# Kernel optimization log

Measured on AMD Instinct MI355X. Metric: run time of the kernel, lower is better.

The kernel has to match this reference:

```python
import jax, jax.numpy as jnp
import numpy as np
import math

DIM = 512
B, T, H, W = 1, 8, 64, 64


def setup_inputs() -> dict:
    key = jax.random.key(0)
    k0, k1, k2 = jax.random.split(key, 3)
    x = jax.random.normal(k0, (B, DIM, T, H, W), dtype=jnp.float32)
    gamma = jnp.ones((DIM,), jnp.float32)                      # RMS_norm gamma (viewed as flat vector)
    w_qkv = jax.random.normal(k1, (3 * DIM, DIM), jnp.float32) * 0.02  # conv1x1 weight (out, in)
    b_qkv = jnp.zeros((3 * DIM,), jnp.float32)
    w_proj = jax.random.normal(k2, (DIM, DIM), jnp.float32) * 0.02     # zero-init in torch; random for a meaningful baseline
    b_proj = jnp.zeros((DIM,), jnp.float32)
    return dict(x=x, gamma=gamma, w_qkv=w_qkv, b_qkv=b_qkv, w_proj=w_proj, b_proj=b_proj)


def reference(x, gamma, w_qkv, b_qkv, w_proj, b_proj):
    b, c, t, h, w = x.shape
    xt = jnp.transpose(x, (0, 2, 3, 4, 1))          # [b, t, h, w, c]
    identity = xt
    y = xt.reshape(b * t, h, w, c)
    # RMS_norm: L2 norm over channels (last dim), clamped, scaled by sqrt(c)*gamma
    norm = jnp.clip(jnp.linalg.norm(y, axis=-1, keepdims=True), 1e-12, None)
    y = y / norm * (c ** 0.5) * gamma
    # 1x1 conv QKV as GEMM over channels
    qkv = jnp.einsum('bhwc,oc->bhwo', y, w_qkv) + b_qkv        # [bt, h, w, 3c]
    qkv = qkv.reshape(b * t, h * w, 1, 3 * c)                  # nh=1 per source rearrange
    q, k, v = jnp.split(qkv, 3, axis=-1)                       # each [bt, hw, 1, c]
    scale = 1.0 / math.sqrt(c)
    # NOTE: hw sits in the batch position (faithful to source); seq len = nh = 1
    attn = jnp.einsum('bsnc,bsmc->bsnm', q, k) * scale         # [bt, hw, 1, 1]
    attn = jax.nn.softmax(attn, axis=-1)                       # trivially 1.0
    o = jnp.einsum('bsnm,bsmc->bsnc', attn, v)                 # == v
    o = o.reshape(b * t, h, w, c)
    o = jnp.einsum('bhwc,oc->bhwo', o, w_proj) + b_proj        # 1x1 proj conv
    o = o.reshape(b, t, h, w, c)
    out = jnp.transpose(o + identity, (0, 4, 1, 2, 3))         # back to [b, c, t, h, w]
    return out
```

## Files before the change

### kernel.cpp

```cpp
#include <hip/hip_runtime.h>

typedef unsigned short ushort_t;
typedef __attribute__((ext_vector_type(8))) short short8;
typedef __attribute__((ext_vector_type(4))) float f32x4;

#define DIMC 512
#define PN   32768
#define SQRTC 22.627416997969522f

__device__ __forceinline__ ushort_t f2bf(float f) {
  unsigned int u = __float_as_uint(f);
  unsigned int r = u + 0x7fffu + ((u >> 16) & 1u);
  return (ushort_t)(r >> 16);
}

__device__ __forceinline__ int kkey(int r) { return (r & 7) ^ ((r >> 2) & 7); }

__device__ __forceinline__ uint4 pack8(float4 a, float4 b) {
  union { ushort_t u[8]; uint4 v; } r;
  r.u[0] = f2bf(a.x); r.u[1] = f2bf(a.y); r.u[2] = f2bf(a.z); r.u[3] = f2bf(a.w);
  r.u[4] = f2bf(b.x); r.u[5] = f2bf(b.y); r.u[6] = f2bf(b.z); r.u[7] = f2bf(b.w);
  return r.v;
}

__global__ __launch_bounds__(256) void k_wgemm(
    const float* __restrict__ wproj,
    const float* __restrict__ wqkv,
    const float* __restrict__ bqkv,
    const float* __restrict__ bproj,
    const float* __restrict__ gamma,
    ushort_t* __restrict__ Mp2,
    float* __restrict__ fb) {
  int bid = blockIdx.x, tid = threadIdx.x;
  if (bid >= 16) {
    int wave = tid >> 6, lane = tid & 63;
    int o = (bid - 16) * 4 + wave;
    float part = 0.f;
#pragma unroll
    for (int i = 0; i < 8; ++i) {
      int k = lane + i * 64;
      part += wproj[o * DIMC + k] * bqkv[1024 + k];
    }
    for (int off = 32; off; off >>= 1) part += __shfl_down(part, off, 64);
    if (lane == 0) fb[o] = part + bproj[o];
    return;
  }

  __shared__ ushort_t As[128 * 64];
  __shared__ ushort_t Bs[128 * 64];
  int c0 = (bid & 3) * 128;
  int o0 = (bid >> 2) * 128;
  int wave = tid >> 6, lane = tid & 63;
  int wo = (wave & 1) * 64, wp = (wave >> 1) * 64;
  int q = lane >> 4, ln = lane & 15;

  f32x4 zero = {0.f, 0.f, 0.f, 0.f};
  f32x4 acc[4][4];
#pragma unroll
  for (int i = 0; i < 4; ++i)
#pragma unroll
    for (int j = 0; j < 4; ++j) acc[i][j] = zero;

  int sr = tid >> 3;
  int sc = tid & 7;
  const float* Ag = wproj + (long)(o0 + sr) * DIMC + sc * 8;
  int kr = tid >> 5;
  int c4 = (tid & 31) * 4;

  for (int kc = 0; kc < DIMC; kc += 64) {
    __syncthreads();
#pragma unroll
    for (int it = 0; it < 4; ++it) {
      int r = sr + it * 32;
      float4 a0 = *(const float4*)(Ag + (long)it * 32 * DIMC + kc);
      float4 a1 = *(const float4*)(Ag + (long)it * 32 * DIMC + kc + 4);
      *(uint4*)(&As[r * 64 + ((sc ^ (r & 7)) * 8)]) = pack8(a0, a1);
    }
#pragma unroll
    for (int ps = 0; ps < 8; ++ps) {
      int k = kc + ps * 8 + kr;
      float4 b = *(const float4*)(wqkv + (long)(1024 + k) * DIMC + c0 + c4);
      char* bsb = (char*)Bs;
      ushort_t e[4] = {f2bf(b.x), f2bf(b.y), f2bf(b.z), f2bf(b.w)};
#pragma unroll
      for (int i = 0; i < 4; ++i) {
        int c = c4 + i;
        *(ushort_t*)(bsb + c * 128 + ((ps ^ kkey(c)) * 16) + kr * 2) = e[i];
      }
    }
    __syncthreads();
#pragma unroll
    for (int ks = 0; ks < 2; ++ks) {
      int cch = ks * 4 + q;
      short8 af[4], bf[4];
#pragma unroll
      for (int mi = 0; mi < 4; ++mi) {
        int row = wo + mi * 16 + ln;
        af[mi] = *(const short8*)(&As[row * 64 + ((cch ^ (row & 7)) * 8)]);
      }
#pragma unroll
      for (int ni = 0; ni < 4; ++ni) {
        int row = wp + ni * 16 + ln;
        bf[ni] = *(const short8*)(&Bs[row * 64 + ((cch ^ kkey(row)) * 8)]);
      }
#pragma unroll
      for (int mi = 0; mi < 4; ++mi)
#pragma unroll
        for (int ni = 0; ni < 4; ++ni)
          acc[mi][ni] = __builtin_amdgcn_mfma_f32_16x16x32_bf16(af[mi], bf[ni], acc[mi][ni], 0, 0, 0);
    }
  }

#pragma unroll
  for (int mi = 0; mi < 4; ++mi) {
    int obase = o0 + wo + mi * 16 + q * 4;
#pragma unroll
    for (int ni = 0; ni < 4; ++ni) {
      int c = c0 + wp + ni * 16 + ln;
      float g = gamma[c];
      int kb2 = c >> 6, ks2 = (c >> 5) & 1, q2 = (c >> 3) & 3, j2 = c & 7;
#pragma unroll
      for (int r = 0; r < 4; ++r) {
        int o = obase + r;
        int w2 = o >> 6, mi2 = (o >> 4) & 3, ln2 = o & 15;
        long idx = (((((long)w2 * 8 + kb2) * 2 + ks2) * 4 + mi2) * 64 + q2 * 16 + ln2) * 8 + j2;
        Mp2[idx] = f2bf(acc[mi][ni][r] * g);
      }
    }
  }
}

__global__ __launch_bounds__(512, 4) void k_fused(
    const float* __restrict__ x,
    const ushort_t* __restrict__ Mp2,
    const float* __restrict__ fb,
    float* __restrict__ out) {
  __shared__ ushort_t xs[8 * 64 * 64];
  __shared__ float red[32 * 65];
  __shared__ float s_sh[64];
  int tid = threadIdx.x;
  long p0 = (long)blockIdx.x * 64;

  int wave = tid >> 6, lane = tid & 63;
  int q = lane >> 4, ln = lane & 15;

  int pl4 = (tid & 15) * 4;
  int kp  = tid >> 4;
  int kl  = kp * 2;
  int ch  = kl >> 3;
  int sub = (kl & 7) * 2;
  const float* xb = x + p0 + pl4;

  const ushort_t* Aw = Mp2 + (long)wave * 32768 + lane * 8;

  float ss0 = 0.f, ss1 = 0.f, ss2 = 0.f, ss3 = 0.f;
  float4 u0, u1;

#define LOADX(KB)                                                  \
  { const float* xp = xb + (long)((KB) * 64 + kl) * PN;            \
    u0 = *(const float4*)(xp);  u1 = *(const float4*)(xp + PN); }

#define SSW(KB)                                                                 \
  { ss0 += u0.x * u0.x + u1.x * u1.x;  ss1 += u0.y * u0.y + u1.y * u1.y;        \
    ss2 += u0.z * u0.z + u1.z * u1.z;  ss3 += u0.w * u0.w + u1.w * u1.w;        \
    unsigned int w0 = (unsigned int)f2bf(u0.x) | ((unsigned int)f2bf(u1.x) << 16); \
    unsigned int w1 = (unsigned int)f2bf(u0.y) | ((unsigned int)f2bf(u1.y) << 16); \
    unsigned int w2 = (unsigned int)f2bf(u0.z) | ((unsigned int)f2bf(u1.z) << 16); \
    unsigned int w3 = (unsigned int)f2bf(u0.w) | ((unsigned int)f2bf(u1.w) << 16); \
    char* bb = (char*)xs + (KB) * 8192;                                         \
    *(unsigned int*)(bb + (pl4 + 0) * 128 + ((ch ^ kkey(pl4 + 0)) * 16) + sub) = w0; \
    *(unsigned int*)(bb + (pl4 + 1) * 128 + ((ch ^ kkey(pl4 + 1)) * 16) + sub) = w1; \
    *(unsigned int*)(bb + (pl4 + 2) * 128 + ((ch ^ kkey(pl4 + 2)) * 16) + sub) = w2; \
    *(unsigned int*)(bb + (pl4 + 3) * 128 + ((ch ^ kkey(pl4 + 3)) * 16) + sub) = w3; }

  f32x4 zero = {0.f, 0.f, 0.f, 0.f};
  f32x4 acc[4][4];
#pragma unroll
  for (int i = 0; i < 4; ++i)
#pragma unroll
    for (int j = 0; j < 4; ++j) acc[i][j] = zero;

  LOADX(0); SSW(0);
  __syncthreads();

#pragma unroll
  for (int kb = 0; kb < 8; ++kb) {
    if (kb < 7) LOADX(kb + 1);
    const char* bbase = (const char*)xs + kb * 8192;
#pragma unroll
    for (int ks = 0; ks < 2; ++ks) {
      short8 af[4], bf[4];
#pragma unroll
      for (int mi = 0; mi < 4; ++mi)
        af[mi] = *(const short8*)(Aw + ((kb * 2 + ks) * 4 + mi) * 512);
      int cch = ks * 4 + q;
#pragma unroll
      for (int ni = 0; ni < 4; ++ni) {
        int row = ni * 16 + ln;
        bf[ni] = *(const short8*)(bbase + row * 128 + ((cch ^ kkey(row)) * 16));
      }
#pragma unroll
      for (int mi = 0; mi < 4; ++mi)
#pragma unroll
        for (int ni = 0; ni < 4; ++ni)
          acc[mi][ni] = __builtin_amdgcn_mfma_f32_16x16x32_bf16(af[mi], bf[ni], acc[mi][ni], 0, 0, 0);
    }
    if (kb < 7) {
      SSW(kb + 1);
      __syncthreads();
    }
  }

  red[kp * 65 + pl4 + 0] = ss0;
  red[kp * 65 + pl4 + 1] = ss1;
  red[kp * 65 + pl4 + 2] = ss2;
  red[kp * 65 + pl4 + 3] = ss3;
  __syncthreads();
  if (tid < 64) {
    float t = 0.f;
#pragma unroll
    for (int g = 0; g < 32; ++g) t += red[g * 65 + tid];
    s_sh[tid] = SQRTC / fmaxf(sqrtf(t), 1e-12f);
  }
  __syncthreads();

  int wo = wave * 64;
#pragma unroll
  for (int mi = 0; mi < 4; ++mi) {
    int obase = wo + mi * 16 + q * 4;
#pragma unroll
    for (int ni = 0; ni < 4; ++ni) {
      int plocal = ni * 16 + ln;
      long p = p0 + plocal;
      float sv = s_sh[plocal];
#pragma unroll
      for (int r = 0; r < 4; ++r) {
        int o = obase + r;
        out[(long)o * PN + p] = x[(long)o * PN + p] + fb[o] + sv * acc[mi][ni][r];
      }
    }
  }
#undef LOADX
#undef SSW
}

extern "C" void kernel_launch(void* const* d_in, const int* in_sizes, int n_in,
                              void* d_out, int out_size, void* d_ws, size_t ws_size,
                              hipStream_t stream) {
  const float* x     = (const float*)d_in[0];
  const float* gamma = (const float*)d_in[1];
  const float* wqkv  = (const float*)d_in[2];
  const float* bqkv  = (const float*)d_in[3];
  const float* wproj = (const float*)d_in[4];
  const float* bproj = (const float*)d_in[5];

  char* ws = (char*)d_ws;
  ushort_t* Mp2 = (ushort_t*)(ws);
  float*    fb  = (float*)(ws + 524288);

  k_wgemm<<<dim3(144), dim3(256), 0, stream>>>(wproj, wqkv, bqkv, bproj, gamma, Mp2, fb);
  k_fused<<<dim3(512), dim3(512), 0, stream>>>(x, Mp2, fb, (float*)d_out);
}
```

Measured before the change: 188.9 us.

## Load full x tile upfront, drop per-chunk barriers, double-buffer weight fragments

The fused kernel now loads the whole 64-pixel by 512-channel x tile into registers in one burst, converts it to bf16 in LDS, and computes the RMS norm before the GEMM loop. This removes the seven per-chunk __syncthreads and the interleaved global loads inside the MFMA loop. Weight fragments are prefetched one k-block ahead into a register double buffer. Register use rises sharply (16 float4 plus 16 short8), so launch bounds drop from 4 to 2 blocks per SM, which lowers occupancy and reduces latency hiding for the memory-bound x read.

```diff
diff --git a/kernel.cpp b/kernel.cpp
--- a/kernel.cpp
+++ b/kernel.cpp
@@ -130,7 +130,7 @@
   }
 }
 
-__global__ __launch_bounds__(512, 4) void k_fused(
+__global__ __launch_bounds__(512, 2) void k_fused(
     const float* __restrict__ x,
     const ushort_t* __restrict__ Mp2,
     const float* __restrict__ fb,
@@ -144,34 +144,57 @@
   int wave = tid >> 6, lane = tid & 63;
   int q = lane >> 4, ln = lane & 15;
 
+  const ushort_t* Aw = Mp2 + (long)wave * 32768 + lane * 8;
+
   int pl4 = (tid & 15) * 4;
-  int kp  = tid >> 4;
-  int kl  = kp * 2;
-  int ch  = kl >> 3;
-  int sub = (kl & 7) * 2;
-  const float* xb = x + p0 + pl4;
-
-  const ushort_t* Aw = Mp2 + (long)wave * 32768 + lane * 8;
+  int kq  = tid >> 4;
+  float4 v[16];
+#pragma unroll
+  for (int sw = 0; sw < 4; ++sw) {
+    const float* xp = x + (long)(kq * 4 + sw * 128) * PN + p0 + pl4;
+#pragma unroll
+    for (int j = 0; j < 4; ++j)
+      v[sw * 4 + j] = *(const float4*)(xp + (long)j * PN);
+  }
+
+  short8 afb[2][8];
+#pragma unroll
+  for (int f = 0; f < 8; ++f) afb[0][f] = *(const short8*)(Aw + f * 512);
 
   float ss0 = 0.f, ss1 = 0.f, ss2 = 0.f, ss3 = 0.f;
-  float4 u0, u1;
-
-#define LOADX(KB)                                                  \
-  { const float* xp = xb + (long)((KB) * 64 + kl) * PN;            \
-    u0 = *(const float4*)(xp);  u1 = *(const float4*)(xp + PN); }
-
-#define SSW(KB)                                                                 \
-  { ss0 += u0.x * u0.x + u1.x * u1.x;  ss1 += u0.y * u0.y + u1.y * u1.y;        \
-    ss2 += u0.z * u0.z + u1.z * u1.z;  ss3 += u0.w * u0.w + u1.w * u1.w;        \
-    unsigned int w0 = (unsigned int)f2bf(u0.x) | ((unsigned int)f2bf(u1.x) << 16); \
-    unsigned int w1 = (unsigned int)f2bf(u0.y) | ((unsigned int)f2bf(u1.y) << 16); \
-    unsigned int w2 = (unsigned int)f2bf(u0.z) | ((unsigned int)f2bf(u1.z) << 16); \
-    unsigned int w3 = (unsigned int)f2bf(u0.w) | ((unsigned int)f2bf(u1.w) << 16); \
-    char* bb = (char*)xs + (KB) * 8192;                                         \
-    *(unsigned int*)(bb + (pl4 + 0) * 128 + ((ch ^ kkey(pl4 + 0)) * 16) + sub) = w0; \
-    *(unsigned int*)(bb + (pl4 + 1) * 128 + ((ch ^ kkey(pl4 + 1)) * 16) + sub) = w1; \
-    *(unsigned int*)(bb + (pl4 + 2) * 128 + ((ch ^ kkey(pl4 + 2)) * 16) + sub) = w2; \
-    *(unsigned int*)(bb + (pl4 + 3) * 128 + ((ch ^ kkey(pl4 + 3)) * 16) + sub) = w3; }
+#pragma unroll
+  for (int sw = 0; sw < 4; ++sw) {
+    int k4 = kq * 4 + sw * 128;
+    float4 v0 = v[sw * 4 + 0], v1 = v[sw * 4 + 1];
+    float4 v2 = v[sw * 4 + 2], v3 = v[sw * 4 + 3];
+    ss0 += v0.x * v0.x + v1.x * v1.x + v2.x * v2.x + v3.x * v3.x;
+    ss1 += v0.y * v0.y + v1.y * v1.y + v2.y * v2.y + v3.y * v3.y;
+    ss2 += v0.z * v0.z + v1.z * v1.z + v2.z * v2.z + v3.z * v3.z;
+    ss3 += v0.w * v0.w + v1.w * v1.w + v2.w * v2.w + v3.w * v3.w;
+    ushort_t t0[4] = {f2bf(v0.x), f2bf(v1.x), f2bf(v2.x), f2bf(v3.x)};
+    ushort_t t1[4] = {f2bf(v0.y), f2bf(v1.y), f2bf(v2.y), f2bf(v3.y)};
+    ushort_t t2[4] = {f2bf(v0.z), f2bf(v1.z), f2bf(v2.z), f2bf(v3.z)};
+    ushort_t t3[4] = {f2bf(v0.w), f2bf(v1.w), f2bf(v2.w), f2bf(v3.w)};
+    char* base = (char*)xs + (k4 >> 6) * 8192;
+    int ch  = (k4 >> 3) & 7;
+    int sub = (k4 & 7) * 2;
+    *(uint2*)(base + (pl4 + 0) * 128 + ((ch ^ kkey(pl4 + 0)) * 16) + sub) = *(const uint2*)t0;
+    *(uint2*)(base + (pl4 + 1) * 128 + ((ch ^ kkey(pl4 + 1)) * 16) + sub) = *(const uint2*)t1;
+    *(uint2*)(base + (pl4 + 2) * 128 + ((ch ^ kkey(pl4 + 2)) * 16) + sub) = *(const uint2*)t2;
+    *(uint2*)(base + (pl4 + 3) * 128 + ((ch ^ kkey(pl4 + 3)) * 16) + sub) = *(const uint2*)t3;
+  }
+  red[kq * 65 + pl4 + 0] = ss0;
+  red[kq * 65 + pl4 + 1] = ss1;
+  red[kq * 65 + pl4 + 2] = ss2;
+  red[kq * 65 + pl4 + 3] = ss3;
+  __syncthreads();
+
+  if (tid < 64) {
+    float t = 0.f;
+#pragma unroll
+    for (int g = 0; g < 32; ++g) t += red[g * 65 + tid];
+    s_sh[tid] = SQRTC / fmaxf(sqrtf(t), 1e-12f);
+  }
 
   f32x4 zero = {0.f, 0.f, 0.f, 0.f};
   f32x4 acc[4][4];
@@ -180,20 +203,18 @@
 #pragma unroll
     for (int j = 0; j < 4; ++j) acc[i][j] = zero;
 
-  LOADX(0); SSW(0);
-  __syncthreads();
-
 #pragma unroll
   for (int kb = 0; kb < 8; ++kb) {
-    if (kb < 7) LOADX(kb + 1);
+    if (kb < 7) {
+#pragma unroll
+      for (int f = 0; f < 8; ++f)
+        afb[(kb + 1) & 1][f] = *(const short8*)(Aw + ((kb + 1) * 8 + f) * 512);
+    }
     const char* bbase = (const char*)xs + kb * 8192;
 #pragma unroll
     for (int ks = 0; ks < 2; ++ks) {
-      short8 af[4], bf[4];
-#pragma unroll
-      for (int mi = 0; mi < 4; ++mi)
-        af[mi] = *(const short8*)(Aw + ((kb * 2 + ks) * 4 + mi) * 512);
       int cch = ks * 4 + q;
+      short8 bf[4];
 #pragma unroll
       for (int ni = 0; ni < 4; ++ni) {
         int row = ni * 16 + ln;
@@ -203,24 +224,9 @@
       for (int mi = 0; mi < 4; ++mi)
 #pragma unroll
         for (int ni = 0; ni < 4; ++ni)
-          acc[mi][ni] = __builtin_amdgcn_mfma_f32_16x16x32_bf16(af[mi], bf[ni], acc[mi][ni], 0, 0, 0);
-    }
-    if (kb < 7) {
-      SSW(kb + 1);
-      __syncthreads();
-    }
-  }
-
-  red[kp * 65 + pl4 + 0] = ss0;
-  red[kp * 65 + pl4 + 1] = ss1;
-  red[kp * 65 + pl4 + 2] = ss2;
-  red[kp * 65 + pl4 + 3] = ss3;
-  __syncthreads();
-  if (tid < 64) {
-    float t = 0.f;
-#pragma unroll
-    for (int g = 0; g < 32; ++g) t += red[g * 65 + tid];
-    s_sh[tid] = SQRTC / fmaxf(sqrtf(t), 1e-12f);
+          acc[mi][ni] = __builtin_amdgcn_mfma_f32_16x16x32_bf16(
+              afb[kb & 1][ks * 4 + mi], bf[ni], acc[mi][ni], 0, 0, 0);
+    }
   }
   __syncthreads();
 
@@ -240,8 +246,6 @@
       }
     }
   }
-#undef LOADX
-#undef SSW
 }
 
 extern "C" void kernel_launch(void* const* d_in, const int* in_sizes, int n_in,
```

After: 171.4 us. 9.3% less time.

## Process two pixel tiles per block, overlapping next tile load with epilogue

Applied to the files above, without the earlier changes.

Each fused block now handles two 64-pixel tiles (grid halved to 256). The kernel loads the whole 512-channel x slab into registers up front, then issues the second tile's loads before the first tile's epilogue stores, so global traffic overlaps compute. A weight fragments are double-buffered in registers across k-blocks. In exchange it uses more registers (launch bounds drop to 2 blocks per CU), and with only 256 blocks on a 256-CU device there is less parallelism to hide latency.

```diff
diff --git a/kernel.cpp b/kernel.cpp
--- a/kernel.cpp
+++ b/kernel.cpp
@@ -130,118 +130,156 @@
   }
 }
 
-__global__ __launch_bounds__(512, 4) void k_fused(
+__global__ __launch_bounds__(512, 2) void k_fused(
     const float* __restrict__ x,
     const ushort_t* __restrict__ Mp2,
     const float* __restrict__ fb,
     float* __restrict__ out) {
   __shared__ ushort_t xs[8 * 64 * 64];
   __shared__ float red[32 * 65];
-  __shared__ float s_sh[64];
+  __shared__ float s_sh[2][64];
   int tid = threadIdx.x;
-  long p0 = (long)blockIdx.x * 64;
+  long pt0 = (long)blockIdx.x * 128;
 
   int wave = tid >> 6, lane = tid & 63;
   int q = lane >> 4, ln = lane & 15;
-
   int pl4 = (tid & 15) * 4;
-  int kp  = tid >> 4;
-  int kl  = kp * 2;
-  int ch  = kl >> 3;
-  int sub = (kl & 7) * 2;
-  const float* xb = x + p0 + pl4;
+  int kq  = tid >> 4;
 
   const ushort_t* Aw = Mp2 + (long)wave * 32768 + lane * 8;
 
-  float ss0 = 0.f, ss1 = 0.f, ss2 = 0.f, ss3 = 0.f;
-  float4 u0, u1;
-
-#define LOADX(KB)                                                  \
-  { const float* xp = xb + (long)((KB) * 64 + kl) * PN;            \
-    u0 = *(const float4*)(xp);  u1 = *(const float4*)(xp + PN); }
-
-#define SSW(KB)                                                                 \
-  { ss0 += u0.x * u0.x + u1.x * u1.x;  ss1 += u0.y * u0.y + u1.y * u1.y;        \
-    ss2 += u0.z * u0.z + u1.z * u1.z;  ss3 += u0.w * u0.w + u1.w * u1.w;        \
-    unsigned int w0 = (unsigned int)f2bf(u0.x) | ((unsigned int)f2bf(u1.x) << 16); \
-    unsigned int w1 = (unsigned int)f2bf(u0.y) | ((unsigned int)f2bf(u1.y) << 16); \
-    unsigned int w2 = (unsigned int)f2bf(u0.z) | ((unsigned int)f2bf(u1.z) << 16); \
-    unsigned int w3 = (unsigned int)f2bf(u0.w) | ((unsigned int)f2bf(u1.w) << 16); \
-    char* bb = (char*)xs + (KB) * 8192;                                         \
-    *(unsigned int*)(bb + (pl4 + 0) * 128 + ((ch ^ kkey(pl4 + 0)) * 16) + sub) = w0; \
-    *(unsigned int*)(bb + (pl4 + 1) * 128 + ((ch ^ kkey(pl4 + 1)) * 16) + sub) = w1; \
-    *(unsigned int*)(bb + (pl4 + 2) * 128 + ((ch ^ kkey(pl4 + 2)) * 16) + sub) = w2; \
-    *(unsigned int*)(bb + (pl4 + 3) * 128 + ((ch ^ kkey(pl4 + 3)) * 16) + sub) = w3; }
+  float4 v[16];
+
+#define LOADV(TB)                                                        \
+  {                                                                      \
+    _Pragma("unroll")                                                    \
+    for (int sw = 0; sw < 4; ++sw) {                                     \
+      const float* xp = x + (long)(kq * 4 + sw * 128) * PN + (TB) + pl4; \
+      _Pragma("unroll")                                                  \
+      for (int j = 0; j < 4; ++j)                                        \
+        v[sw * 4 + j] = *(const float4*)(xp + (long)j * PN);             \
+    }                                                                    \
+  }
+
+#define PROCESSV()                                                                     \
+  {                                                                                    \
+    float ss0 = 0.f, ss1 = 0.f, ss2 = 0.f, ss3 = 0.f;                                  \
+    _Pragma("unroll")                                                                  \
+    for (int sw = 0; sw < 4; ++sw) {                                                   \
+      int k4 = kq * 4 + sw * 128;                                                      \
+      float4 v0 = v[sw * 4 + 0], v1 = v[sw * 4 + 1];                                   \
+      float4 v2 = v[sw * 4 + 2], v3 = v[sw * 4 + 3];                                   \
+      ss0 += v0.x * v0.x + v1.x * v1.x + v2.x * v2.x + v3.x * v3.x;                    \
+      ss1 += v0.y * v0.y + v1.y * v1.y + v2.y * v2.y + v3.y * v3.y;                    \
+      ss2 += v0.z * v0.z + v1.z * v1.z + v2.z * v2.z + v3.z * v3.z;                    \
+      ss3 += v0.w * v0.w + v1.w * v1.w + v2.w * v2.w + v3.w * v3.w;                    \
+      ushort_t t0[4] = {f2bf(v0.x), f2bf(v1.x), f2bf(v2.x), f2bf(v3.x)};               \
+      ushort_t t1[4] = {f2bf(v0.y), f2bf(v1.y), f2bf(v2.y), f2bf(v3.y)};               \
+      ushort_t t2[4] = {f2bf(v0.z), f2bf(v1.z), f2bf(v2.z), f2bf(v3.z)};               \
+      ushort_t t3[4] = {f2bf(v0.w), f2bf(v1.w), f2bf(v2.w), f2bf(v3.w)};               \
+      char* base = (char*)xs + (k4 >> 6) * 8192;                                       \
+      int ch  = (k4 >> 3) & 7;                                                         \
+      int sub = (k4 & 7) * 2;                                                          \
+      *(uint2*)(base + (pl4 + 0) * 128 + ((ch ^ kkey(pl4 + 0)) * 16) + sub) = *(const uint2*)t0; \
+      *(uint2*)(base + (pl4 + 1) * 128 + ((ch ^ kkey(pl4 + 1)) * 16) + sub) = *(const uint2*)t1; \
+      *(uint2*)(base + (pl4 + 2) * 128 + ((ch ^ kkey(pl4 + 2)) * 16) + sub) = *(const uint2*)t2; \
+      *(uint2*)(base + (pl4 + 3) * 128 + ((ch ^ kkey(pl4 + 3)) * 16) + sub) = *(const uint2*)t3; \
+    }                                                                                  \
+    red[kq * 65 + pl4 + 0] = ss0;                                                      \
+    red[kq * 65 + pl4 + 1] = ss1;                                                      \
+    red[kq * 65 + pl4 + 2] = ss2;                                                      \
+    red[kq * 65 + pl4 + 3] = ss3;                                                      \
+  }
+
+#define SREDUCE(SI)                                          \
+  if (tid < 64) {                                            \
+    float t = 0.f;                                           \
+    _Pragma("unroll")                                        \
+    for (int g = 0; g < 32; ++g) t += red[g * 65 + tid];     \
+    s_sh[SI][tid] = SQRTC / fmaxf(sqrtf(t), 1e-12f);         \
+  }
 
   f32x4 zero = {0.f, 0.f, 0.f, 0.f};
   f32x4 acc[4][4];
-#pragma unroll
-  for (int i = 0; i < 4; ++i)
-#pragma unroll
-    for (int j = 0; j < 4; ++j) acc[i][j] = zero;
-
-  LOADX(0); SSW(0);
+  short8 afb[2][8];
+
+#define GEMMT()                                                                   \
+  {                                                                               \
+    _Pragma("unroll")                                                             \
+    for (int i = 0; i < 4; ++i)                                                   \
+      _Pragma("unroll")                                                           \
+      for (int j = 0; j < 4; ++j) acc[i][j] = zero;                               \
+    _Pragma("unroll")                                                             \
+    for (int f = 0; f < 8; ++f) afb[0][f] = *(const short8*)(Aw + f * 512);       \
+    _Pragma("unroll")                                                             \
+    for (int kb = 0; kb < 8; ++kb) {                                              \
+      if (kb < 7) {                                                               \
+        _Pragma("unroll")                                                         \
+        for (int f = 0; f < 8; ++f)                                               \
+          afb[(kb + 1) & 1][f] = *(const short8*)(Aw + ((kb + 1) * 8 + f) * 512); \
+      }                                                                           \
+      const char* bbase = (const char*)xs + kb * 8192;                            \
+      _Pragma("unroll")                                                           \
+      for (int ks = 0; ks < 2; ++ks) {                                            \
+        int cch = ks * 4 + q;                                                     \
+        short8 bfr[4];                                                            \
+        _Pragma("unroll")                                                         \
+        for (int ni = 0; ni < 4; ++ni) {                                          \
+          int row = ni * 16 + ln;                                                 \
+          bfr[ni] = *(const short8*)(bbase + row * 128 + ((cch ^ kkey(row)) * 16)); \
+        }                                                                         \
+        _Pragma("unroll")                                                         \
+        for (int mi = 0; mi < 4; ++mi)                                            \
+          _Pragma("unroll")                                                       \
+          for (int ni = 0; ni < 4; ++ni)                                          \
+            acc[mi][ni] = __builtin_amdgcn_mfma_f32_16x16x32_bf16(                \
+                afb[kb & 1][ks * 4 + mi], bfr[ni], acc[mi][ni], 0, 0, 0);         \
+      }                                                                           \
+    }                                                                             \
+  }
+
+#define EPI(TB, SI)                                                       \
+  {                                                                       \
+    int wo = wave * 64;                                                   \
+    _Pragma("unroll")                                                     \
+    for (int mi = 0; mi < 4; ++mi) {                                      \
+      int obase = wo + mi * 16 + q * 4;                                   \
+      _Pragma("unroll")                                                   \
+      for (int ni = 0; ni < 4; ++ni) {                                    \
+        int plocal = ni * 16 + ln;                                        \
+        long p = (TB) + plocal;                                           \
+        float sv = s_sh[SI][plocal];                                      \
+        _Pragma("unroll")                                                 \
+        for (int r = 0; r < 4; ++r) {                                     \
+          int o = obase + r;                                              \
+          out[(long)o * PN + p] = x[(long)o * PN + p] + fb[o] + sv * acc[mi][ni][r]; \
+        }                                                                 \
+      }                                                                   \
+    }                                                                     \
+  }
+
+  LOADV(pt0);
+  PROCESSV();
   __syncthreads();
-
-#pragma unroll
-  for (int kb = 0; kb < 8; ++kb) {
-    if (kb < 7) LOADX(kb + 1);
-    const char* bbase = (const char*)xs + kb * 8192;
-#pragma unroll
-    for (int ks = 0; ks < 2; ++ks) {
-      short8 af[4], bf[4];
-#pragma unroll
-      for (int mi = 0; mi < 4; ++mi)
-        af[mi] = *(const short8*)(Aw + ((kb * 2 + ks) * 4 + mi) * 512);
-      int cch = ks * 4 + q;
-#pragma unroll
-      for (int ni = 0; ni < 4; ++ni) {
-        int row = ni * 16 + ln;
-        bf[ni] = *(const short8*)(bbase + row * 128 + ((cch ^ kkey(row)) * 16));
-      }
-#pragma unroll
-      for (int mi = 0; mi < 4; ++mi)
-#pragma unroll
-        for (int ni = 0; ni < 4; ++ni)
-          acc[mi][ni] = __builtin_amdgcn_mfma_f32_16x16x32_bf16(af[mi], bf[ni], acc[mi][ni], 0, 0, 0);
-    }
-    if (kb < 7) {
-      SSW(kb + 1);
-      __syncthreads();
-    }
-  }
-
-  red[kp * 65 + pl4 + 0] = ss0;
-  red[kp * 65 + pl4 + 1] = ss1;
-  red[kp * 65 + pl4 + 2] = ss2;
-  red[kp * 65 + pl4 + 3] = ss3;
+  SREDUCE(0);
+  GEMMT();
   __syncthreads();
-  if (tid < 64) {
-    float t = 0.f;
-#pragma unroll
-    for (int g = 0; g < 32; ++g) t += red[g * 65 + tid];
-    s_sh[tid] = SQRTC / fmaxf(sqrtf(t), 1e-12f);
-  }
+
+  LOADV(pt0 + 64);
+  EPI(pt0, 0);
+  PROCESSV();
   __syncthreads();
-
-  int wo = wave * 64;
-#pragma unroll
-  for (int mi = 0; mi < 4; ++mi) {
-    int obase = wo + mi * 16 + q * 4;
-#pragma unroll
-    for (int ni = 0; ni < 4; ++ni) {
-      int plocal = ni * 16 + ln;
-      long p = p0 + plocal;
-      float sv = s_sh[plocal];
-#pragma unroll
-      for (int r = 0; r < 4; ++r) {
-        int o = obase + r;
-        out[(long)o * PN + p] = x[(long)o * PN + p] + fb[o] + sv * acc[mi][ni][r];
-      }
-    }
-  }
-#undef LOADX
-#undef SSW
+  SREDUCE(1);
+
+  GEMMT();
+  __syncthreads();
+  EPI(pt0 + 64, 1);
+
+#undef LOADV
+#undef PROCESSV
+#undef SREDUCE
+#undef GEMMT
+#undef EPI
 }
 
 extern "C" void kernel_launch(void* const* d_in, const int* in_sizes, int n_in,
@@ -259,5 +297,5 @@
   float*    fb  = (float*)(ws + 524288);
 
   k_wgemm<<<dim3(144), dim3(256), 0, stream>>>(wproj, wqkv, bqkv, bproj, gamma, Mp2, fb);
-  k_fused<<<dim3(512), dim3(512), 0, stream>>>(x, Mp2, fb, (float*)d_out);
-}
+  k_fused<<<dim3(256), dim3(512), 0, stream>>>(x, Mp2, fb, (float*)d_out);
+}
```

New measurement: 210.1 us. +11.2%, slower.
